# Optimization experiments

Hardware: AMD Instinct MI355X
Metric: run time of the kernel (lower is better)

Reference implementation:

```python
import jax, jax.numpy as jnp
import numpy as np

NODE_DIM = 256
HID = 128
EDGE_DIM = 128
NUM_BINS = 22
MAX_LEN = 2056
TOTAL_FEATS = HID * 3 + NUM_BINS * 2 + 2


def get_index_embedding(indices, embed_size, max_len):
    # sinusoidal index embedding as in RiboFlow utils
    K = jnp.arange(embed_size // 2, dtype=jnp.float32)
    ang = indices[..., None].astype(jnp.float32) * jnp.pi / (max_len ** (2.0 * K / embed_size))
    return jnp.concatenate([jnp.sin(ang), jnp.cos(ang)], axis=-1)


def calc_distogram(pos, min_bin, max_bin, num_bins):
    # pos: [B, N, 3] -> one-hot distogram [B, N, N, num_bins]
    d = jnp.linalg.norm(pos[:, :, None, :] - pos[:, None, :, :], axis=-1)[..., None]
    lower = jnp.linspace(min_bin, max_bin, num_bins)
    upper = jnp.concatenate([lower[1:], jnp.array([1e8], dtype=jnp.float32)])
    return ((d > lower) & (d < upper)).astype(jnp.float32)


def cross_concat(f):
    # f: [B, N, D] -> [B, N, N, 2D] via row/col tiling
    B, N, D = f.shape
    return jnp.concatenate([
        jnp.broadcast_to(f[:, :, None, :], (B, N, N, D)),
        jnp.broadcast_to(f[:, None, :, :], (B, N, N, D)),
    ], axis=-1)


def _linear_params(key, fi, fo):
    s = 1.0 / np.sqrt(fi)
    kw, kb = jax.random.split(key)
    W = jax.random.uniform(kw, (fi, fo), jnp.float32, -s, s)
    b = jax.random.uniform(kb, (fo,), jnp.float32, -s, s)
    return W, b


def setup_inputs() -> dict:
    key = jax.random.key(0)
    ks = jax.random.split(key, 12)
    B, N = 1, 512
    inp = {
        'node_features': jax.random.normal(ks[0], (B, N, NODE_DIM), jnp.float32),
        'trans': jax.random.normal(ks[1], (B, N, 3), jnp.float32) * 10.0,
        'sc_trans': jax.random.normal(ks[2], (B, N, 3), jnp.float32) * 10.0,
        'edge_mask': jnp.ones((B, N, N), jnp.float32),
        'flow_mask': (jax.random.uniform(ks[4], (B, N)) > 0.5).astype(jnp.float32),
    }
    inp['W_n2e'], inp['b_n2e'] = _linear_params(ks[5], NODE_DIM, HID)
    inp['W_rp'], inp['b_rp'] = _linear_params(ks[6], HID, HID)
    inp['W1'], inp['b1'] = _linear_params(ks[7], TOTAL_FEATS, EDGE_DIM)
    inp['W2'], inp['b2'] = _linear_params(ks[8], EDGE_DIM, EDGE_DIM)
    inp['W3'], inp['b3'] = _linear_params(ks[9], EDGE_DIM, EDGE_DIM)
    inp['ln_g'] = jnp.ones((EDGE_DIM,), jnp.float32)
    inp['ln_b'] = jnp.zeros((EDGE_DIM,), jnp.float32)
    return inp


def reference(node_features, trans, sc_trans, edge_mask, flow_mask,
              W_n2e, b_n2e, W_rp, b_rp, W1, b1, W2, b2, W3, b3, ln_g, ln_b):
    B, N, _ = node_features.shape
    # node -> edge projection, then cross-concat tiling: [B,N,N,2*HID]
    n2e = node_features @ W_n2e + b_n2e
    pair_node_feats = cross_concat(n2e)
    # relative position sinusoidal embedding + linear: [B,N,N,HID]
    seq = jnp.arange(N, dtype=jnp.float32)
    relpos = jnp.broadcast_to(seq[None, :, None] - seq[None, None, :], (B, N, N))
    relpos_feats = get_index_embedding(relpos, HID, MAX_LEN) @ W_rp + b_rp
    # distograms: [B,N,N,NUM_BINS] each
    dist_feats = calc_distogram(trans, 0.001, 20.0, NUM_BINS)
    sc_feats = calc_distogram(sc_trans, 0.001, 20.0, NUM_BINS)
    # flow mask pair features: [B,N,N,2]
    flow_feat = cross_concat(flow_mask[..., None])
    feats = jnp.concatenate([pair_node_feats, relpos_feats, dist_feats, sc_feats, flow_feat], axis=-1)
    # 3-layer MLP + LayerNorm
    h = jax.nn.relu(feats @ W1 + b1)
    h = jax.nn.relu(h @ W2 + b2)
    h = h @ W3 + b3
    mu = jnp.mean(h, axis=-1, keepdims=True)
    var = jnp.var(h, axis=-1, keepdims=True)
    h = (h - mu) * jax.lax.rsqrt(var + 1e-5) * ln_g + ln_b
    return h * edge_mask[..., None]
```

## Files before the change

### kernel.cpp

```cpp
#include <hip/hip_runtime.h>


using bf16x8 = __attribute__((ext_vector_type(8))) short;
using f32x4  = __attribute__((ext_vector_type(4))) float;

__device__ __forceinline__ unsigned short f2bf(float f) {
    unsigned int u;
    __builtin_memcpy(&u, &f, 4);
    unsigned int r = (u + 0x7fffu + ((u >> 16) & 1u)) >> 16;
    return (unsigned short)r;
}

__device__ __forceinline__ unsigned int cvt_pk_bf16(float lo, float hi) {
    unsigned int r;
    asm("v_cvt_pk_bf16_f32 %0, %1, %2" : "=v"(r) : "v"(lo), "v"(hi));
    return r;
}

__global__ void pre_all(const float* __restrict__ nf,
                        const float* __restrict__ Wn2e,
                        const float* __restrict__ bn2e,
                        const float* __restrict__ W1,
                        const float* __restrict__ b1,
                        const float* __restrict__ flow,
                        const float* __restrict__ Wrp,
                        const float* __restrict__ brp,
                        const float* __restrict__ W2,
                        const float* __restrict__ W3,
                        float* __restrict__ A, float* __restrict__ Bv,
                        float* __restrict__ Rm,
                        short* __restrict__ W2b, short* __restrict__ W3b)
{
    __shared__ float s0[256];
    __shared__ float s1[128];
    const int bid = blockIdx.x;
    const int m = threadIdx.x;

    if (bid < 512) {
        const int i = bid;
        s0[m]       = nf[i * 256 + m];
        s0[m + 128] = nf[i * 256 + 128 + m];
        __syncthreads();
        float acc = bn2e[m];
        for (int k = 0; k < 256; k++) acc += s0[k] * Wn2e[k * 128 + m];
        s1[m] = acc;
        __syncthreads();
        const float fl = flow[i];
        float aA = b1[m] + fl * W1[428 * 128 + m];
        float aB =         fl * W1[429 * 128 + m];
        for (int k = 0; k < 128; k++) {
            const float s = s1[k];
            aA += s * W1[k * 128 + m];
            aB += s * W1[(128 + k) * 128 + m];
        }
        A[i * 128 + m]  = aA;
        Bv[i * 128 + m] = aB;
    } else if (bid < 1535) {
        const int dix = bid - 512;
        const float d = (float)(dix - 511);
        const int K = m & 63;
        const float denom = powf(2056.0f, (float)K * (1.0f / 64.0f));
        const float ang = d * 3.14159265358979323846f / denom;
        s0[m] = (m < 64) ? sinf(ang) : cosf(ang);
        __syncthreads();
        float acc = brp[m];
        for (int k = 0; k < 128; k++) acc += s0[k] * Wrp[k * 128 + m];
        s1[m] = acc;
        __syncthreads();
        float acc2 = 0.0f;
        for (int k = 0; k < 128; k++) acc2 += s1[k] * W1[(256 + k) * 128 + m];
        Rm[dix * 128 + m] = acc2;
    } else {
        const int t = (bid - 1535) * 128 + m;
        for (int h = 0; h < 2; h++) {
            const int idx = t + h * 8192;
            const int k = idx >> 7, n = idx & 127;
            const int dst = ((k >> 3) * 128 + n) * 8 + (k & 7);
            W2b[dst] = (short)f2bf(W2[idx]);
            W3b[dst] = (short)f2bf(W3[idx]);
        }
    }
}

__global__ __launch_bounds__(512, 2) void edge_main(
    const float* __restrict__ trans,
    const float* __restrict__ sctrans,
    const float* __restrict__ emask,
    const float* __restrict__ W1,
    const short* __restrict__ W2b,
    const float* __restrict__ b2,
    const short* __restrict__ W3b,
    const float* __restrict__ b3,
    const float* __restrict__ lng,
    const float* __restrict__ lnb,
    const float* __restrict__ A,
    const float* __restrict__ Bv,
    const float* __restrict__ Rm,
    float* __restrict__ out)
{
    __shared__ __align__(16) short W2L[16384];
    __shared__ __align__(16) short W3L[16384];
    __shared__ __align__(16) short h2w[8 * 16 * 140];
    __shared__ __align__(16) float As[128];
    __shared__ int binsD[256];
    __shared__ int binsS[256];

    const int tid = threadIdx.x;
    const int i  = blockIdx.x >> 1;
    const int j0 = (blockIdx.x & 1) << 8;

    for (int r = 0; r < 4; r++) {
        const int off = (r * 512 + tid) * 16;
        __builtin_amdgcn_global_load_lds(
            (const __attribute__((address_space(1))) void*)((const char*)W2b + off),
            (__attribute__((address_space(3))) void*)((char*)W2L + off), 16, 0, 0);
        __builtin_amdgcn_global_load_lds(
            (const __attribute__((address_space(1))) void*)((const char*)W3b + off),
            (__attribute__((address_space(3))) void*)((char*)W3L + off), 16, 0, 0);
    }

    if (tid < 128) As[tid] = A[i * 128 + tid];

    {
        const int p = tid & 255;
        const float* P = (tid < 256) ? trans : sctrans;
        const int j = j0 + p;
        const float dx = __fsub_rn(P[i * 3 + 0], P[j * 3 + 0]);
        const float dy = __fsub_rn(P[i * 3 + 1], P[j * 3 + 1]);
        const float dz = __fsub_rn(P[i * 3 + 2], P[j * 3 + 2]);
        const float d2 = __fadd_rn(__fadd_rn(__fmul_rn(dx, dx), __fmul_rn(dy, dy)),
                                   __fmul_rn(dz, dz));
        const double dd = (double)sqrtf(d2);
        const double step = (20.0 - 0.001) / 21.0;
        int bin = -1;
        for (int b = 0; b < 22; b++) {
            const double lo = (b == 21) ? 20.0 : __dadd_rn(0.001, __dmul_rn((double)b, step));
            const double up = (b == 20) ? 20.0 :
                              ((b == 21) ? 1e8 : __dadd_rn(0.001, __dmul_rn((double)(b + 1), step)));
            if (dd > lo && dd < up) bin = b;
        }
        if (tid < 256) binsD[p] = bin; else binsS[p] = bin;
    }
    __syncthreads();

    const int w = tid >> 6;
    const int l = tid & 63;
    const int q = l >> 4;
    const int ln16 = l & 15;

    bf16x8 af[2][4];
    for (int mt = 0; mt < 2; mt++) {
        const int p = 32 * w + mt * 16 + ln16;
        const int j = j0 + p;
        const int didx = i - j + 511;
        const int bD = binsD[p], bS = binsS[p];
        const float sD = bD >= 0 ? 1.0f : 0.0f;
        const float sS = bS >= 0 ? 1.0f : 0.0f;
        const int rD = 384 + (bD >= 0 ? bD : 0);
        const int rS = 406 + (bS >= 0 ? bS : 0);
        const float* __restrict__ BvR = &Bv[j * 128];
        const float* __restrict__ RmR = &Rm[didx * 128];
        const float* __restrict__ WdR = &W1[rD * 128];
        const float* __restrict__ WsR = &W1[rS * 128];
        for (int kb = 0; kb < 4; kb++) {
            const int f0 = kb * 32 + q * 8;
            const f32x4 bv0 = *(const f32x4*)&BvR[f0];
            const f32x4 bv1 = *(const f32x4*)&BvR[f0 + 4];
            const f32x4 r0  = *(const f32x4*)&RmR[f0];
            const f32x4 r1  = *(const f32x4*)&RmR[f0 + 4];
            const f32x4 a0  = *(const f32x4*)&As[f0];
            const f32x4 a1  = *(const f32x4*)&As[f0 + 4];
            const f32x4 w0  = *(const f32x4*)&WdR[f0];
            const f32x4 w1  = *(const f32x4*)&WdR[f0 + 4];
            const f32x4 s0  = *(const f32x4*)&WsR[f0];
            const f32x4 s1  = *(const f32x4*)&WsR[f0 + 4];
            float h[8];
            for (int e = 0; e < 4; e++) {
                h[e]     = fmaxf(a0[e] + bv0[e] + r0[e] + sD * w0[e] + sS * s0[e], 0.0f);
                h[e + 4] = fmaxf(a1[e] + bv1[e] + r1[e] + sD * w1[e] + sS * s1[e], 0.0f);
            }
            union { unsigned int u[4]; bf16x8 v; } cv;
            cv.u[0] = cvt_pk_bf16(h[0], h[1]);
            cv.u[1] = cvt_pk_bf16(h[2], h[3]);
            cv.u[2] = cvt_pk_bf16(h[4], h[5]);
            cv.u[3] = cvt_pk_bf16(h[6], h[7]);
            af[mt][kb] = cv.v;
        }
    }

    const f32x4 vzero = {0.0f, 0.0f, 0.0f, 0.0f};
    short* const h2p = &h2w[w * 16 * 140];

    float b2v[8], b3v[8], gv[8], bbv[8];
    for (int nb = 0; nb < 8; nb++) {
        const int n = nb * 16 + ln16;
        b2v[nb] = b2[n]; b3v[nb] = b3[n]; gv[nb] = lng[n]; bbv[nb] = lnb[n];
    }

    for (int mt = 0; mt < 2; mt++) {
        for (int nb = 0; nb < 8; nb++) {
            f32x4 acc = vzero;
            for (int kb = 0; kb < 4; kb++) {
                const bf16x8 bfrg = *(const bf16x8*)&W2L[((kb * 4 + q) * 128 + nb * 16 + ln16) * 8];
                acc = __builtin_amdgcn_mfma_f32_16x16x32_bf16(af[mt][kb], bfrg, acc, 0, 0, 0);
            }
            for (int rg = 0; rg < 4; rg++) {
                const float v = fmaxf(acc[rg] + b2v[nb], 0.0f);
                h2p[(q * 4 + rg) * 140 + nb * 16 + ln16] = (short)cvt_pk_bf16(v, v);
            }
        }

        bf16x8 a3[4];
        for (int kb = 0; kb < 4; kb++)
            a3[kb] = *(const bf16x8*)&h2p[ln16 * 140 + q * 8 + kb * 32];

        f32x4 acc3[8];
        for (int nb = 0; nb < 8; nb++) acc3[nb] = vzero;
        for (int nb = 0; nb < 8; nb++)
            for (int kb = 0; kb < 4; kb++) {
                const bf16x8 bfrg = *(const bf16x8*)&W3L[((kb * 4 + q) * 128 + nb * 16 + ln16) * 8];
                acc3[nb] = __builtin_amdgcn_mfma_f32_16x16x32_bf16(a3[kb], bfrg, acc3[nb], 0, 0, 0);
            }

        for (int rg = 0; rg < 4; rg++) {
            float v[8];
            float s = 0.0f;
            for (int nb = 0; nb < 8; nb++) { v[nb] = acc3[nb][rg] + b3v[nb]; s += v[nb]; }
            for (int mm = 1; mm < 16; mm <<= 1) s += __shfl_xor(s, mm, 64);
            const float mu = s * (1.0f / 128.0f);
            float ss = 0.0f;
            for (int nb = 0; nb < 8; nb++) { const float dv = v[nb] - mu; ss += dv * dv; }
            for (int mm = 1; mm < 16; mm <<= 1) ss += __shfl_xor(ss, mm, 64);
            const float rstd = rsqrtf(ss * (1.0f / 128.0f) + 1e-5f);
            const int p = 32 * w + mt * 16 + q * 4 + rg;
            const int j = j0 + p;
            const float msk = emask[i * 512 + j];
            const int obase = (i * 512 + j) * 128;
            for (int nb = 0; nb < 8; nb++) {
                const float o = ((v[nb] - mu) * rstd * gv[nb] + bbv[nb]) * msk;
                out[obase + nb * 16 + ln16] = o;
            }
        }
    }
}

extern "C" void kernel_launch(void* const* d_in, const int* in_sizes, int n_in,
                              void* d_out, int out_size, void* d_ws, size_t ws_size,
                              hipStream_t stream)
{
    const float* nf    = (const float*)d_in[0];
    const float* trans = (const float*)d_in[1];
    const float* sctr  = (const float*)d_in[2];
    const float* emask = (const float*)d_in[3];
    const float* flow  = (const float*)d_in[4];
    const float* Wn2e  = (const float*)d_in[5];
    const float* bn2e  = (const float*)d_in[6];
    const float* Wrp   = (const float*)d_in[7];
    const float* brp   = (const float*)d_in[8];
    const float* W1    = (const float*)d_in[9];
    const float* b1    = (const float*)d_in[10];
    const float* W2    = (const float*)d_in[11];
    const float* b2    = (const float*)d_in[12];
    const float* W3    = (const float*)d_in[13];
    const float* b3    = (const float*)d_in[14];
    const float* lng   = (const float*)d_in[15];
    const float* lnb   = (const float*)d_in[16];

    float* ws = (float*)d_ws;
    float* A   = ws;
    float* Bv  = ws + 512 * 128;
    float* Rm  = ws + 2 * 512 * 128;
    short* W2b = (short*)(ws + 262016);
    short* W3b = (short*)(ws + 270208);
    float* out = (float*)d_out;

    pre_all<<<1599, 128, 0, stream>>>(nf, Wn2e, bn2e, W1, b1, flow, Wrp, brp,
                                      W2, W3, A, Bv, Rm, W2b, W3b);
    edge_main<<<1024, 512, 0, stream>>>(trans, sctr, emask, W1, W2b, b2, W3b, b3,
                                        lng, lnb, A, Bv, Rm, out);
}
```

Measured before the change: 259.0 us.

## Swap MFMA operand order, pass layer-2 output via ds_bpermute, vectorize LN stores

The edge kernel now computes the transposed products (weights as the A operand), so each lane holds one edge row's features across columns. The layer-2 activations are reshuffled into layer-3 B fragments with ds_bpermute instead of a shared-memory staging buffer. LayerNorm then reduces with only two cross-lane shuffles and writes float4 stores. The h2w shared buffer is removed and launch bounds rise to 4 blocks per CU to allow more occupancy, and the precompute kernel's dot products use multiple accumulators. Risks include register pressure under the tighter launch bound and extra bpermute traffic.

```diff
diff --git a/kernel.cpp b/kernel.cpp
--- a/kernel.cpp
+++ b/kernel.cpp
@@ -41,20 +41,28 @@
         s0[m]       = nf[i * 256 + m];
         s0[m + 128] = nf[i * 256 + 128 + m];
         __syncthreads();
-        float acc = bn2e[m];
-        for (int k = 0; k < 256; k++) acc += s0[k] * Wn2e[k * 128 + m];
-        s1[m] = acc;
+        float c0 = 0.f, c1 = 0.f, c2 = 0.f, c3 = 0.f;
+        #pragma unroll 4
+        for (int k = 0; k < 256; k += 4) {
+            c0 += s0[k + 0] * Wn2e[(k + 0) * 128 + m];
+            c1 += s0[k + 1] * Wn2e[(k + 1) * 128 + m];
+            c2 += s0[k + 2] * Wn2e[(k + 2) * 128 + m];
+            c3 += s0[k + 3] * Wn2e[(k + 3) * 128 + m];
+        }
+        s1[m] = bn2e[m] + ((c0 + c1) + (c2 + c3));
         __syncthreads();
         const float fl = flow[i];
-        float aA = b1[m] + fl * W1[428 * 128 + m];
-        float aB =         fl * W1[429 * 128 + m];
-        for (int k = 0; k < 128; k++) {
-            const float s = s1[k];
-            aA += s * W1[k * 128 + m];
-            aB += s * W1[(128 + k) * 128 + m];
-        }
-        A[i * 128 + m]  = aA;
-        Bv[i * 128 + m] = aB;
+        float aA0 = b1[m] + fl * W1[428 * 128 + m], aA1 = 0.f;
+        float aB0 =         fl * W1[429 * 128 + m], aB1 = 0.f;
+        #pragma unroll 4
+        for (int k = 0; k < 128; k += 2) {
+            aA0 += s1[k]     * W1[(k) * 128 + m];
+            aA1 += s1[k + 1] * W1[(k + 1) * 128 + m];
+            aB0 += s1[k]     * W1[(128 + k) * 128 + m];
+            aB1 += s1[k + 1] * W1[(129 + k) * 128 + m];
+        }
+        A[i * 128 + m]  = aA0 + aA1;
+        Bv[i * 128 + m] = aB0 + aB1;
     } else if (bid < 1535) {
         const int dix = bid - 512;
         const float d = (float)(dix - 511);
@@ -63,13 +71,25 @@
         const float ang = d * 3.14159265358979323846f / denom;
         s0[m] = (m < 64) ? sinf(ang) : cosf(ang);
         __syncthreads();
-        float acc = brp[m];
-        for (int k = 0; k < 128; k++) acc += s0[k] * Wrp[k * 128 + m];
-        s1[m] = acc;
+        float c0 = 0.f, c1 = 0.f, c2 = 0.f, c3 = 0.f;
+        #pragma unroll 4
+        for (int k = 0; k < 128; k += 4) {
+            c0 += s0[k + 0] * Wrp[(k + 0) * 128 + m];
+            c1 += s0[k + 1] * Wrp[(k + 1) * 128 + m];
+            c2 += s0[k + 2] * Wrp[(k + 2) * 128 + m];
+            c3 += s0[k + 3] * Wrp[(k + 3) * 128 + m];
+        }
+        s1[m] = brp[m] + ((c0 + c1) + (c2 + c3));
         __syncthreads();
-        float acc2 = 0.0f;
-        for (int k = 0; k < 128; k++) acc2 += s1[k] * W1[(256 + k) * 128 + m];
-        Rm[dix * 128 + m] = acc2;
+        c0 = 0.f; c1 = 0.f; c2 = 0.f; c3 = 0.f;
+        #pragma unroll 4
+        for (int k = 0; k < 128; k += 4) {
+            c0 += s1[k + 0] * W1[(256 + k) * 128 + m];
+            c1 += s1[k + 1] * W1[(257 + k) * 128 + m];
+            c2 += s1[k + 2] * W1[(258 + k) * 128 + m];
+            c3 += s1[k + 3] * W1[(259 + k) * 128 + m];
+        }
+        Rm[dix * 128 + m] = (c0 + c1) + (c2 + c3);
     } else {
         const int t = (bid - 1535) * 128 + m;
         for (int h = 0; h < 2; h++) {
@@ -82,7 +102,7 @@
     }
 }
 
-__global__ __launch_bounds__(512, 2) void edge_main(
+__global__ __launch_bounds__(512, 4) void edge_main(
     const float* __restrict__ trans,
     const float* __restrict__ sctrans,
     const float* __restrict__ emask,
@@ -100,7 +120,6 @@
 {
     __shared__ __align__(16) short W2L[16384];
     __shared__ __align__(16) short W3L[16384];
-    __shared__ __align__(16) short h2w[8 * 16 * 140];
     __shared__ __align__(16) float As[128];
     __shared__ int binsD[256];
     __shared__ int binsS[256];
@@ -148,98 +167,131 @@
     const int q = l >> 4;
     const int ln16 = l & 15;
 
-    bf16x8 af[2][4];
+    const f32x4 vzero = {0.0f, 0.0f, 0.0f, 0.0f};
+    const int laA = (((q & 1) * 2) * 16 + ln16) * 4;
+    const int laB = laA + 64;
+    const bool selHi = (q >> 1) != 0;
+
     for (int mt = 0; mt < 2; mt++) {
         const int p = 32 * w + mt * 16 + ln16;
         const int j = j0 + p;
-        const int didx = i - j + 511;
-        const int bD = binsD[p], bS = binsS[p];
-        const float sD = bD >= 0 ? 1.0f : 0.0f;
-        const float sS = bS >= 0 ? 1.0f : 0.0f;
-        const int rD = 384 + (bD >= 0 ? bD : 0);
-        const int rS = 406 + (bS >= 0 ? bS : 0);
-        const float* __restrict__ BvR = &Bv[j * 128];
-        const float* __restrict__ RmR = &Rm[didx * 128];
-        const float* __restrict__ WdR = &W1[rD * 128];
-        const float* __restrict__ WsR = &W1[rS * 128];
+
+        bf16x8 af[4];
+        {
+            const int didx = i - j + 511;
+            const int bD = binsD[p], bS = binsS[p];
+            const float sD = bD >= 0 ? 1.0f : 0.0f;
+            const float sS = bS >= 0 ? 1.0f : 0.0f;
+            const int rD = 384 + (bD >= 0 ? bD : 0);
+            const int rS = 406 + (bS >= 0 ? bS : 0);
+            const float* __restrict__ BvR = &Bv[j * 128];
+            const float* __restrict__ RmR = &Rm[didx * 128];
+            const float* __restrict__ WdR = &W1[rD * 128];
+            const float* __restrict__ WsR = &W1[rS * 128];
+            #pragma unroll
+            for (int kb = 0; kb < 4; kb++) {
+                const int f0 = kb * 32 + q * 8;
+                const f32x4 bv0 = *(const f32x4*)&BvR[f0];
+                const f32x4 bv1 = *(const f32x4*)&BvR[f0 + 4];
+                const f32x4 r0  = *(const f32x4*)&RmR[f0];
+                const f32x4 r1  = *(const f32x4*)&RmR[f0 + 4];
+                const f32x4 a0  = *(const f32x4*)&As[f0];
+                const f32x4 a1  = *(const f32x4*)&As[f0 + 4];
+                const f32x4 w0  = *(const f32x4*)&WdR[f0];
+                const f32x4 w1  = *(const f32x4*)&WdR[f0 + 4];
+                const f32x4 s0  = *(const f32x4*)&WsR[f0];
+                const f32x4 s1  = *(const f32x4*)&WsR[f0 + 4];
+                float h[8];
+                #pragma unroll
+                for (int e = 0; e < 4; e++) {
+                    h[e]     = fmaxf(a0[e] + bv0[e] + r0[e] + sD * w0[e] + sS * s0[e], 0.0f);
+                    h[e + 4] = fmaxf(a1[e] + bv1[e] + r1[e] + sD * w1[e] + sS * s1[e], 0.0f);
+                }
+                union { unsigned int u[4]; bf16x8 v; } cv;
+                cv.u[0] = cvt_pk_bf16(h[0], h[1]);
+                cv.u[1] = cvt_pk_bf16(h[2], h[3]);
+                cv.u[2] = cvt_pk_bf16(h[4], h[5]);
+                cv.u[3] = cvt_pk_bf16(h[6], h[7]);
+                af[kb] = cv.v;
+            }
+        }
+
+        unsigned int P[8][2];
+        #pragma unroll
+        for (int nt = 0; nt < 8; nt++) {
+            f32x4 acc2 = vzero;
+            #pragma unroll
+            for (int kb = 0; kb < 4; kb++) {
+                const bf16x8 wf = *(const bf16x8*)&W2L[((kb * 4 + q) * 128 + nt * 16 + ln16) * 8];
+                acc2 = __builtin_amdgcn_mfma_f32_16x16x32_bf16(wf, af[kb], acc2, 0, 0, 0);
+            }
+            const f32x4 b2c = *(const f32x4*)&b2[nt * 16 + q * 4];
+            P[nt][0] = cvt_pk_bf16(fmaxf(acc2[0] + b2c[0], 0.0f),
+                                   fmaxf(acc2[1] + b2c[1], 0.0f));
+            P[nt][1] = cvt_pk_bf16(fmaxf(acc2[2] + b2c[2], 0.0f),
+                                   fmaxf(acc2[3] + b2c[3], 0.0f));
+        }
+
+        f32x4 acc3[8];
+        #pragma unroll
+        for (int nt = 0; nt < 8; nt++) acc3[nt] = vzero;
+        #pragma unroll
         for (int kb = 0; kb < 4; kb++) {
-            const int f0 = kb * 32 + q * 8;
-            const f32x4 bv0 = *(const f32x4*)&BvR[f0];
-            const f32x4 bv1 = *(const f32x4*)&BvR[f0 + 4];
-            const f32x4 r0  = *(const f32x4*)&RmR[f0];
-            const f32x4 r1  = *(const f32x4*)&RmR[f0 + 4];
-            const f32x4 a0  = *(const f32x4*)&As[f0];
-            const f32x4 a1  = *(const f32x4*)&As[f0 + 4];
-            const f32x4 w0  = *(const f32x4*)&WdR[f0];
-            const f32x4 w1  = *(const f32x4*)&WdR[f0 + 4];
-            const f32x4 s0  = *(const f32x4*)&WsR[f0];
-            const f32x4 s1  = *(const f32x4*)&WsR[f0 + 4];
-            float h[8];
-            for (int e = 0; e < 4; e++) {
-                h[e]     = fmaxf(a0[e] + bv0[e] + r0[e] + sD * w0[e] + sS * s0[e], 0.0f);
-                h[e + 4] = fmaxf(a1[e] + bv1[e] + r1[e] + sD * w1[e] + sS * s1[e], 0.0f);
-            }
-            union { unsigned int u[4]; bf16x8 v; } cv;
-            cv.u[0] = cvt_pk_bf16(h[0], h[1]);
-            cv.u[1] = cvt_pk_bf16(h[2], h[3]);
-            cv.u[2] = cvt_pk_bf16(h[4], h[5]);
-            cv.u[3] = cvt_pk_bf16(h[6], h[7]);
-            af[mt][kb] = cv.v;
-        }
-    }
-
-    const f32x4 vzero = {0.0f, 0.0f, 0.0f, 0.0f};
-    short* const h2p = &h2w[w * 16 * 140];
-
-    float b2v[8], b3v[8], gv[8], bbv[8];
-    for (int nb = 0; nb < 8; nb++) {
-        const int n = nb * 16 + ln16;
-        b2v[nb] = b2[n]; b3v[nb] = b3[n]; gv[nb] = lng[n]; bbv[nb] = lnb[n];
-    }
-
-    for (int mt = 0; mt < 2; mt++) {
-        for (int nb = 0; nb < 8; nb++) {
-            f32x4 acc = vzero;
-            for (int kb = 0; kb < 4; kb++) {
-                const bf16x8 bfrg = *(const bf16x8*)&W2L[((kb * 4 + q) * 128 + nb * 16 + ln16) * 8];
-                acc = __builtin_amdgcn_mfma_f32_16x16x32_bf16(af[mt][kb], bfrg, acc, 0, 0, 0);
-            }
+            const int r0a = __builtin_amdgcn_ds_bpermute(laA, (int)P[2 * kb][0]);
+            const int r1a = __builtin_amdgcn_ds_bpermute(laA, (int)P[2 * kb][1]);
+            const int r2a = __builtin_amdgcn_ds_bpermute(laB, (int)P[2 * kb][0]);
+            const int r3a = __builtin_amdgcn_ds_bpermute(laB, (int)P[2 * kb][1]);
+            const int r0b = __builtin_amdgcn_ds_bpermute(laA, (int)P[2 * kb + 1][0]);
+            const int r1b = __builtin_amdgcn_ds_bpermute(laA, (int)P[2 * kb + 1][1]);
+            const int r2b = __builtin_amdgcn_ds_bpermute(laB, (int)P[2 * kb + 1][0]);
+            const int r3b = __builtin_amdgcn_ds_bpermute(laB, (int)P[2 * kb + 1][1]);
+            union { unsigned int u[4]; bf16x8 v; } bf;
+            bf.u[0] = (unsigned int)(selHi ? r0b : r0a);
+            bf.u[1] = (unsigned int)(selHi ? r1b : r1a);
+            bf.u[2] = (unsigned int)(selHi ? r2b : r2a);
+            bf.u[3] = (unsigned int)(selHi ? r3b : r3a);
+            #pragma unroll
+            for (int nt = 0; nt < 8; nt++) {
+                const bf16x8 wf = *(const bf16x8*)&W3L[((kb * 4 + q) * 128 + nt * 16 + ln16) * 8];
+                acc3[nt] = __builtin_amdgcn_mfma_f32_16x16x32_bf16(wf, bf.v, acc3[nt], 0, 0, 0);
+            }
+        }
+
+        float s = 0.0f;
+        #pragma unroll
+        for (int nt = 0; nt < 8; nt++) {
+            const f32x4 b3c = *(const f32x4*)&b3[nt * 16 + q * 4];
+            #pragma unroll
             for (int rg = 0; rg < 4; rg++) {
-                const float v = fmaxf(acc[rg] + b2v[nb], 0.0f);
-                h2p[(q * 4 + rg) * 140 + nb * 16 + ln16] = (short)cvt_pk_bf16(v, v);
-            }
-        }
-
-        bf16x8 a3[4];
-        for (int kb = 0; kb < 4; kb++)
-            a3[kb] = *(const bf16x8*)&h2p[ln16 * 140 + q * 8 + kb * 32];
-
-        f32x4 acc3[8];
-        for (int nb = 0; nb < 8; nb++) acc3[nb] = vzero;
-        for (int nb = 0; nb < 8; nb++)
-            for (int kb = 0; kb < 4; kb++) {
-                const bf16x8 bfrg = *(const bf16x8*)&W3L[((kb * 4 + q) * 128 + nb * 16 + ln16) * 8];
-                acc3[nb] = __builtin_amdgcn_mfma_f32_16x16x32_bf16(a3[kb], bfrg, acc3[nb], 0, 0, 0);
-            }
-
-        for (int rg = 0; rg < 4; rg++) {
-            float v[8];
-            float s = 0.0f;
-            for (int nb = 0; nb < 8; nb++) { v[nb] = acc3[nb][rg] + b3v[nb]; s += v[nb]; }
-            for (int mm = 1; mm < 16; mm <<= 1) s += __shfl_xor(s, mm, 64);
-            const float mu = s * (1.0f / 128.0f);
-            float ss = 0.0f;
-            for (int nb = 0; nb < 8; nb++) { const float dv = v[nb] - mu; ss += dv * dv; }
-            for (int mm = 1; mm < 16; mm <<= 1) ss += __shfl_xor(ss, mm, 64);
-            const float rstd = rsqrtf(ss * (1.0f / 128.0f) + 1e-5f);
-            const int p = 32 * w + mt * 16 + q * 4 + rg;
-            const int j = j0 + p;
-            const float msk = emask[i * 512 + j];
-            const int obase = (i * 512 + j) * 128;
-            for (int nb = 0; nb < 8; nb++) {
-                const float o = ((v[nb] - mu) * rstd * gv[nb] + bbv[nb]) * msk;
-                out[obase + nb * 16 + ln16] = o;
-            }
+                acc3[nt][rg] += b3c[rg];
+                s += acc3[nt][rg];
+            }
+        }
+        s += __shfl_xor(s, 16, 64);
+        s += __shfl_xor(s, 32, 64);
+        const float mu = s * (1.0f / 128.0f);
+        float ss = 0.0f;
+        #pragma unroll
+        for (int nt = 0; nt < 8; nt++)
+            #pragma unroll
+            for (int rg = 0; rg < 4; rg++) {
+                const float dv = acc3[nt][rg] - mu;
+                ss += dv * dv;
+            }
+        ss += __shfl_xor(ss, 16, 64);
+        ss += __shfl_xor(ss, 32, 64);
+        const float rstd = rsqrtf(ss * (1.0f / 128.0f) + 1e-5f);
+        const float msk = emask[i * 512 + j];
+        float* __restrict__ orow = &out[(i * 512 + j) * 128];
+        #pragma unroll
+        for (int nt = 0; nt < 8; nt++) {
+            const f32x4 gc = *(const f32x4*)&lng[nt * 16 + q * 4];
+            const f32x4 bc = *(const f32x4*)&lnb[nt * 16 + q * 4];
+            f32x4 o;
+            #pragma unroll
+            for (int rg = 0; rg < 4; rg++)
+                o[rg] = ((acc3[nt][rg] - mu) * rstd * gc[rg] + bc[rg]) * msk;
+            *(f32x4*)&orow[nt * 16 + q * 4] = o;
         }
     }
 }
```

After: 251.5 us. -2.9%, faster.
